# Performance work log

Measured on AMD Instinct MI355X. Metric: run time of the kernel, lower is better.

Reference implementation:

```python
import jax, jax.numpy as jnp
import numpy as np

N_PILLARS_X = 512
N_PILLARS_Y = 512
N_POINTS = 1_000_000
C_GRID = 64
C_PC = 64


def setup_inputs() -> dict:
    key = jax.random.key(0)
    k1, k2, k3, k4, k5, k6, k7 = jax.random.split(key, 7)
    grid_flow_embeddings = jax.random.normal(k1, (C_GRID, N_PILLARS_X, N_PILLARS_Y), dtype=jnp.float32)
    point_cloud = jax.random.normal(k2, (N_POINTS, C_PC), dtype=jnp.float32)
    grid_indices = jax.random.randint(k3, (N_POINTS,), 0, N_PILLARS_X * N_PILLARS_Y, dtype=jnp.int64)
    Y_w = jax.random.normal(k4, (32, 128), dtype=jnp.float32) * 0.05
    Y_b = jax.random.normal(k5, (32,), dtype=jnp.float32) * 0.05
    Z_w = jax.random.normal(k6, (3, 32), dtype=jnp.float32) * 0.05
    Z_b = jax.random.normal(k7, (3,), dtype=jnp.float32) * 0.05
    return {
        "grid_flow_embeddings": grid_flow_embeddings,
        "point_cloud": point_cloud,
        "grid_indices": grid_indices,
        "Y_w": Y_w,
        "Y_b": Y_b,
        "Z_w": Z_w,
        "Z_b": Z_b,
    }


def reference(grid_flow_embeddings, point_cloud, grid_indices, Y_w, Y_b, Z_w, Z_b):
    C = grid_flow_embeddings.shape[0]
    # (C, X, Y) -> (X*Y, C): the sparse one-hot matmul is exactly a row gather
    grid_flat = grid_flow_embeddings.reshape(C, -1).T  # [X*Y, C]
    point_embeddings = jnp.take(grid_flat, grid_indices, axis=0)  # [N, C]
    full = jnp.concatenate([point_embeddings, point_cloud], axis=1)  # [N, 128]
    h = full @ Y_w.T + Y_b  # [N, 32]
    out = h @ Z_w.T + Z_b   # [N, 3]
    return out
```

## Files before the change

### kernel.cpp

```cpp
#include <hip/hip_runtime.h>
#include <stdint.h>
#include <stddef.h>

#define NCELLS (512 * 512)
#define CG 64
#define CPC 64
#define CIN 128
#define CH 32
#define COUT 3


typedef float f32x4 __attribute__((ext_vector_type(4)));

__device__ inline f32x4 nt_load4(const float* p) {
    return __builtin_nontemporal_load((const f32x4*)p);
}
__device__ inline unsigned int pack2_bf16_rne(float a, float b) {
    unsigned int ua = __float_as_uint(a);
    unsigned int ub = __float_as_uint(b);
    ua = (ua + 0x7fffu + ((ua >> 16) & 1u)) >> 16;
    ub = (ub + 0x7fffu + ((ub >> 16) & 1u)) >> 16;
    return ua | (ub << 16);
}
__device__ inline float bf16_lo(unsigned int v) { return __uint_as_float(v << 16); }
__device__ inline float bf16_hi(unsigned int v) { return __uint_as_float(v & 0xffff0000u); }

__global__ void __launch_bounds__(256)
gz_kernel(const float* __restrict__ grid,
          const float* __restrict__ Yw,
          const float* __restrict__ Yb,
          const float* __restrict__ Zw,
          const float* __restrict__ Zb,
          uint2* __restrict__ GZ8) {
    __shared__ float4 sW[CG];
    __shared__ float  sB[3];
    const int t = threadIdx.x;

    if (t < CG) {
        float w0 = 0.f, w1 = 0.f, w2 = 0.f;
#pragma unroll
        for (int j = 0; j < CH; ++j) {
            float y = Yw[j * CIN + t];
            w0 = fmaf(Zw[0 * CH + j], y, w0);
            w1 = fmaf(Zw[1 * CH + j], y, w1);
            w2 = fmaf(Zw[2 * CH + j], y, w2);
        }
        sW[t] = make_float4(w0, w1, w2, 0.f);
    } else if (t == CG) {
        float b0 = Zb[0], b1 = Zb[1], b2 = Zb[2];
#pragma unroll
        for (int j = 0; j < CH; ++j) {
            float y = Yb[j];
            b0 = fmaf(Zw[0 * CH + j], y, b0);
            b1 = fmaf(Zw[1 * CH + j], y, b1);
            b2 = fmaf(Zw[2 * CH + j], y, b2);
        }
        sB[0] = b0; sB[1] = b1; sB[2] = b2;
    }
    __syncthreads();

    const int p = blockIdx.x * 256 + t;
    float a0 = sB[0], a1 = sB[1], a2 = sB[2];

#pragma unroll 8
    for (int c = 0; c < CG; ++c) {
        float g = __builtin_nontemporal_load(grid + (size_t)c * NCELLS + p);
        float4 w = sW[c];
        a0 = fmaf(w.x, g, a0);
        a1 = fmaf(w.y, g, a1);
        a2 = fmaf(w.z, g, a2);
    }
    GZ8[p] = make_uint2(pack2_bf16_rne(a0, a1), pack2_bf16_rne(a2, 0.f));
}

__global__ void __launch_bounds__(256)
main_kernel(const uint2* __restrict__ GZ8,
            const float* __restrict__ pc,
            const void* __restrict__ idx_raw,
            const float* __restrict__ Yw,
            const float* __restrict__ Zw,
            float* __restrict__ out, int N) {
    __shared__ float4 sW[CG];
    __shared__ int    sFlag;
    const int t = threadIdx.x;

    if (t < CG) {
        float w0 = 0.f, w1 = 0.f, w2 = 0.f;
#pragma unroll
        for (int j = 0; j < CH; ++j) {
            float y = Yw[j * CIN + CG + t];
            w0 = fmaf(Zw[0 * CH + j], y, w0);
            w1 = fmaf(Zw[1 * CH + j], y, w1);
            w2 = fmaf(Zw[2 * CH + j], y, w2);
        }
        sW[t] = make_float4(w0, w1, w2, 0.f);
    } else if (t == CG) {
        int is64 = 1;
        for (int i = 0; i < 8; ++i) {
            if (((const unsigned long long*)idx_raw)[i] >= (unsigned long long)NCELLS) {
                is64 = 0; break;
            }
        }
        sFlag = is64;
    }
    __syncthreads();

    const int ls = t & 7;
    const int tid = blockIdx.x * blockDim.x + t;
    const int gstride = (gridDim.x * blockDim.x) >> 3;
    const int is64 = sFlag;

    const float4 wA0 = sW[4 * ls + 0];
    const float4 wA1 = sW[4 * ls + 1];
    const float4 wA2 = sW[4 * ls + 2];
    const float4 wA3 = sW[4 * ls + 3];
    const float4 wB0 = sW[32 + 4 * ls + 0];
    const float4 wB1 = sW[32 + 4 * ls + 1];
    const float4 wB2 = sW[32 + 4 * ls + 2];
    const float4 wB3 = sW[32 + 4 * ls + 3];

#pragma unroll 2
    for (int p = tid >> 3; p < N; p += gstride) {
        uint2 gz8 = make_uint2(0u, 0u);
        if (ls == 0) {
            int idx;
            if (is64) idx = (int)__builtin_nontemporal_load((const long long*)idx_raw + p);
            else      idx = __builtin_nontemporal_load((const int*)idx_raw + p);
            gz8 = GZ8[idx];
        }

        const float* prow = pc + (size_t)p * CPC;
        f32x4 x0 = nt_load4(prow + 4 * ls);
        f32x4 x1 = nt_load4(prow + 32 + 4 * ls);

        float a0, a1, a2;
        a0 = wA0.x * x0.x;            a1 = wA0.y * x0.x;            a2 = wA0.z * x0.x;
        a0 = fmaf(wA1.x, x0.y, a0);   a1 = fmaf(wA1.y, x0.y, a1);   a2 = fmaf(wA1.z, x0.y, a2);
        a0 = fmaf(wA2.x, x0.z, a0);   a1 = fmaf(wA2.y, x0.z, a1);   a2 = fmaf(wA2.z, x0.z, a2);
        a0 = fmaf(wA3.x, x0.w, a0);   a1 = fmaf(wA3.y, x0.w, a1);   a2 = fmaf(wA3.z, x0.w, a2);
        a0 = fmaf(wB0.x, x1.x, a0);   a1 = fmaf(wB0.y, x1.x, a1);   a2 = fmaf(wB0.z, x1.x, a2);
        a0 = fmaf(wB1.x, x1.y, a0);   a1 = fmaf(wB1.y, x1.y, a1);   a2 = fmaf(wB1.z, x1.y, a2);
        a0 = fmaf(wB2.x, x1.z, a0);   a1 = fmaf(wB2.y, x1.z, a1);   a2 = fmaf(wB2.z, x1.z, a2);
        a0 = fmaf(wB3.x, x1.w, a0);   a1 = fmaf(wB3.y, x1.w, a1);   a2 = fmaf(wB3.z, x1.w, a2);

#pragma unroll
        for (int m = 1; m < 8; m <<= 1) {
            a0 += __shfl_xor(a0, m, 8);
            a1 += __shfl_xor(a1, m, 8);
            a2 += __shfl_xor(a2, m, 8);
        }

        if (ls == 0) {
            float* o = out + (size_t)p * COUT;
            __builtin_nontemporal_store(a0 + bf16_lo(gz8.x), o + 0);
            __builtin_nontemporal_store(a1 + bf16_hi(gz8.x), o + 1);
            __builtin_nontemporal_store(a2 + bf16_lo(gz8.y), o + 2);
        }
    }
}

__global__ void __launch_bounds__(256)
direct_kernel(const float* __restrict__ grid,
              const float* __restrict__ pc,
              const void* __restrict__ idx_raw,
              const float* __restrict__ Yw, const float* __restrict__ Yb,
              const float* __restrict__ Zw, const float* __restrict__ Zb,
              float* __restrict__ out, int N) {
    int i = blockIdx.x * blockDim.x + threadIdx.x;
    if (i >= N) return;
    int idx = (int)(((const long long*)idx_raw)[i]);

    float h[CH];
#pragma unroll
    for (int j = 0; j < CH; ++j) h[j] = Yb[j];
    for (int c = 0; c < CG; ++c) {
        float g = grid[(size_t)c * NCELLS + idx];
#pragma unroll
        for (int j = 0; j < CH; ++j) h[j] = fmaf(Yw[j * CIN + c], g, h[j]);
    }
    const float4* pcp = (const float4*)(pc + (size_t)i * CPC);
#pragma unroll 2
    for (int c4 = 0; c4 < CPC / 4; ++c4) {
        float4 x = pcp[c4];
#pragma unroll
        for (int j = 0; j < CH; ++j) {
            const float* w = Yw + j * CIN + CG + c4 * 4;
            h[j] = fmaf(w[0], x.x, h[j]); h[j] = fmaf(w[1], x.y, h[j]);
            h[j] = fmaf(w[2], x.z, h[j]); h[j] = fmaf(w[3], x.w, h[j]);
        }
    }
#pragma unroll
    for (int t = 0; t < COUT; ++t) {
        float a = Zb[t];
#pragma unroll
        for (int j = 0; j < CH; ++j) a = fmaf(Zw[t * CH + j], h[j], a);
        out[(size_t)i * COUT + t] = a;
    }
}

extern "C" void kernel_launch(void* const* d_in, const int* in_sizes, int n_in,
                              void* d_out, int out_size, void* d_ws, size_t ws_size,
                              hipStream_t stream) {
    const float* grid = (const float*)d_in[0];
    const float* pc   = (const float*)d_in[1];
    const void*  idx  = d_in[2];
    const float* Yw   = (const float*)d_in[3];
    const float* Yb   = (const float*)d_in[4];
    const float* Zw   = (const float*)d_in[5];
    const float* Zb   = (const float*)d_in[6];
    float* out = (float*)d_out;
    const int N = in_sizes[2];

    const size_t GZ_bytes = (size_t)NCELLS * sizeof(uint2);

    if (ws_size >= GZ_bytes && N >= 16) {
        uint2* GZ8 = (uint2*)d_ws;
        gz_kernel<<<NCELLS / 256, 256, 0, stream>>>(grid, Yw, Yb, Zw, Zb, GZ8);
        main_kernel<<<4096, 256, 0, stream>>>(GZ8, pc, idx, Yw, Zw, out, N);
    } else {
        const int threads = 256;
        direct_kernel<<<(N + threads - 1) / threads, threads, 0, stream>>>(
            grid, pc, idx, Yw, Yb, Zw, Zb, out, N);
    }
}
```

Measured before the change: 80.81 us.

## Process 64 points per wave with all lanes loading indices and gathering

Restructures main_kernel so each wavefront handles 64 consecutive points: every lane loads one index and one GZ8 entry, then eight 8-lane groups loop over eight points each, reducing by shuffle and keeping the result for its own lane. This replaces the scheme where only one lane in eight did the index load, gather and store, so index loads and output stores become fully coalesced and all lanes issue the gathers. The grid is also halved to 2048 blocks. The cost is an unrolled 8-iteration inner loop with more live registers and shuffles per point, plus bounds handling for a partial last wave.

New measurement: 67.85 us (median of 2 runs). 1.19x faster.

```diff
diff --git a/kernel.cpp b/kernel.cpp
--- a/kernel.cpp
+++ b/kernel.cpp
@@ -105,9 +105,9 @@
     }
     __syncthreads();
 
-    const int ls = t & 7;
-    const int tid = blockIdx.x * blockDim.x + t;
-    const int gstride = (gridDim.x * blockDim.x) >> 3;
+    const int ls  = t & 7;
+    const int l63 = t & 63;
+    const int gw8 = l63 & ~7;
     const int is64 = sFlag;
 
     const float4 wA0 = sW[4 * ls + 0];
@@ -119,42 +119,60 @@
     const float4 wB2 = sW[32 + 4 * ls + 2];
     const float4 wB3 = sW[32 + 4 * ls + 3];
 
-#pragma unroll 2
-    for (int p = tid >> 3; p < N; p += gstride) {
+    const long long wave_id = (long long)blockIdx.x * (blockDim.x >> 6) + (t >> 6);
+    const long long nwaves  = (long long)gridDim.x * (blockDim.x >> 6);
+
+    for (long long wbase = wave_id * 64; wbase < N; wbase += nwaves * 64) {
+        const long long pm = wbase + l63;
+        const bool full = (wbase + 64 <= N);
+
         uint2 gz8 = make_uint2(0u, 0u);
-        if (ls == 0) {
+        if (full || pm < N) {
             int idx;
-            if (is64) idx = (int)__builtin_nontemporal_load((const long long*)idx_raw + p);
-            else      idx = __builtin_nontemporal_load((const int*)idx_raw + p);
+            if (is64) idx = (int)__builtin_nontemporal_load((const long long*)idx_raw + pm);
+            else      idx = __builtin_nontemporal_load((const int*)idx_raw + pm);
             gz8 = GZ8[idx];
         }
 
-        const float* prow = pc + (size_t)p * CPC;
-        f32x4 x0 = nt_load4(prow + 4 * ls);
-        f32x4 x1 = nt_load4(prow + 32 + 4 * ls);
-
-        float a0, a1, a2;
-        a0 = wA0.x * x0.x;            a1 = wA0.y * x0.x;            a2 = wA0.z * x0.x;
-        a0 = fmaf(wA1.x, x0.y, a0);   a1 = fmaf(wA1.y, x0.y, a1);   a2 = fmaf(wA1.z, x0.y, a2);
-        a0 = fmaf(wA2.x, x0.z, a0);   a1 = fmaf(wA2.y, x0.z, a1);   a2 = fmaf(wA2.z, x0.z, a2);
-        a0 = fmaf(wA3.x, x0.w, a0);   a1 = fmaf(wA3.y, x0.w, a1);   a2 = fmaf(wA3.z, x0.w, a2);
-        a0 = fmaf(wB0.x, x1.x, a0);   a1 = fmaf(wB0.y, x1.x, a1);   a2 = fmaf(wB0.z, x1.x, a2);
-        a0 = fmaf(wB1.x, x1.y, a0);   a1 = fmaf(wB1.y, x1.y, a1);   a2 = fmaf(wB1.z, x1.y, a2);
-        a0 = fmaf(wB2.x, x1.z, a0);   a1 = fmaf(wB2.y, x1.z, a1);   a2 = fmaf(wB2.z, x1.z, a2);
-        a0 = fmaf(wB3.x, x1.w, a0);   a1 = fmaf(wB3.y, x1.w, a1);   a2 = fmaf(wB3.z, x1.w, a2);
-
-#pragma unroll
-        for (int m = 1; m < 8; m <<= 1) {
-            a0 += __shfl_xor(a0, m, 8);
-            a1 += __shfl_xor(a1, m, 8);
-            a2 += __shfl_xor(a2, m, 8);
-        }
-
-        if (ls == 0) {
-            float* o = out + (size_t)p * COUT;
-            __builtin_nontemporal_store(a0 + bf16_lo(gz8.x), o + 0);
-            __builtin_nontemporal_store(a1 + bf16_hi(gz8.x), o + 1);
-            __builtin_nontemporal_store(a2 + bf16_lo(gz8.y), o + 2);
+        float r0 = 0.f, r1 = 0.f, r2 = 0.f;
+
+#pragma unroll
+        for (int k = 0; k < 8; ++k) {
+            const long long pk = wbase + gw8 + k;
+            f32x4 x0, x1;
+            if (full || pk < N) {
+                const float* prow = pc + (size_t)pk * CPC;
+                x0 = nt_load4(prow + 4 * ls);
+                x1 = nt_load4(prow + 32 + 4 * ls);
+            } else {
+                x0 = (f32x4)0.f; x1 = (f32x4)0.f;
+            }
+
+            float a0, a1, a2;
+            a0 = wA0.x * x0.x;            a1 = wA0.y * x0.x;            a2 = wA0.z * x0.x;
+            a0 = fmaf(wA1.x, x0.y, a0);   a1 = fmaf(wA1.y, x0.y, a1);   a2 = fmaf(wA1.z, x0.y, a2);
+            a0 = fmaf(wA2.x, x0.z, a0);   a1 = fmaf(wA2.y, x0.z, a1);   a2 = fmaf(wA2.z, x0.z, a2);
+            a0 = fmaf(wA3.x, x0.w, a0);   a1 = fmaf(wA3.y, x0.w, a1);   a2 = fmaf(wA3.z, x0.w, a2);
+            a0 = fmaf(wB0.x, x1.x, a0);   a1 = fmaf(wB0.y, x1.x, a1);   a2 = fmaf(wB0.z, x1.x, a2);
+            a0 = fmaf(wB1.x, x1.y, a0);   a1 = fmaf(wB1.y, x1.y, a1);   a2 = fmaf(wB1.z, x1.y, a2);
+            a0 = fmaf(wB2.x, x1.z, a0);   a1 = fmaf(wB2.y, x1.z, a1);   a2 = fmaf(wB2.z, x1.z, a2);
+            a0 = fmaf(wB3.x, x1.w, a0);   a1 = fmaf(wB3.y, x1.w, a1);   a2 = fmaf(wB3.z, x1.w, a2);
+
+#pragma unroll
+            for (int m = 1; m < 8; m <<= 1) {
+                a0 += __shfl_xor(a0, m, 8);
+                a1 += __shfl_xor(a1, m, 8);
+                a2 += __shfl_xor(a2, m, 8);
+            }
+
+            if (ls == k) { r0 = a0; r1 = a1; r2 = a2; }
+        }
+
+        if (full || pm < N) {
+            float* o = out + (size_t)pm * COUT;
+            __builtin_nontemporal_store(r0 + bf16_lo(gz8.x), o + 0);
+            __builtin_nontemporal_store(r1 + bf16_hi(gz8.x), o + 1);
+            __builtin_nontemporal_store(r2 + bf16_lo(gz8.y), o + 2);
         }
     }
 }
@@ -216,7 +234,7 @@
     if (ws_size >= GZ_bytes && N >= 16) {
         uint2* GZ8 = (uint2*)d_ws;
         gz_kernel<<<NCELLS / 256, 256, 0, stream>>>(grid, Yw, Yb, Zw, Zb, GZ8);
-        main_kernel<<<4096, 256, 0, stream>>>(GZ8, pc, idx, Yw, Zw, out, N);
+        main_kernel<<<2048, 256, 0, stream>>>(GZ8, pc, idx, Yw, Zw, out, N);
     } else {
         const int threads = 256;
         direct_kernel<<<(N + threads - 1) / threads, threads, 0, stream>>>(
```
